# Optimization experiments

Measured on AMD Instinct MI355X. Metric: run time of the kernel, lower is better.

Reference implementation:

```python
import jax, jax.numpy as jnp
import numpy as np

N = 50000      # nodes
E = 400000     # edges (before self-loops)
DIN = 128
HID = 128
HEADS = 4
DOUT = 64
NEG_SLOPE = 0.2  # PyG GATConv default


def setup_inputs() -> dict:
    key = jax.random.key(0)
    ks = jax.random.split(key, 14)

    def w(k, shape, fan_in):
        return jax.random.normal(k, shape, dtype=jnp.float32) * (1.0 / np.sqrt(fan_in))

    x = jax.random.normal(ks[0], (N, DIN), dtype=jnp.float32)
    edge_index = jax.random.randint(ks[1], (2, E), 0, N, dtype=jnp.int32)

    # layer 1: DIN -> HEADS*HID (concat)
    W1 = w(ks[2], (DIN, HEADS * HID), DIN)
    a_src1 = w(ks[3], (HEADS, HID), HID)
    a_dst1 = w(ks[4], (HEADS, HID), HID)
    b1 = jnp.zeros((HEADS * HID,), jnp.float32)
    # layer 2: HEADS*HID -> HEADS*HID (concat)
    W2 = w(ks[5], (HEADS * HID, HEADS * HID), HEADS * HID)
    a_src2 = w(ks[6], (HEADS, HID), HID)
    a_dst2 = w(ks[7], (HEADS, HID), HID)
    b2 = jnp.zeros((HEADS * HID,), jnp.float32)
    # layer 3: HEADS*HID -> DOUT, heads=1, concat=False (mean)
    W3 = w(ks[8], (HEADS * HID, DOUT), HEADS * HID)
    a_src3 = w(ks[9], (1, DOUT), DOUT)
    a_dst3 = w(ks[10], (1, DOUT), DOUT)
    b3 = jnp.zeros((DOUT,), jnp.float32)

    return dict(x=x, edge_index=edge_index,
                W1=W1, a_src1=a_src1, a_dst1=a_dst1, b1=b1,
                W2=W2, a_src2=a_src2, a_dst2=a_dst2, b2=b2,
                W3=W3, a_src3=a_src3, a_dst3=a_dst3, b3=b3)


def _gat_layer(x, src, dst, W, a_src, a_dst, n):
    """One GATConv (eval mode, self-loops already in src/dst). Returns [n, H, C]."""
    H, C = a_src.shape
    h = (x @ W).reshape(n, H, C)                        # projected features
    alpha_s = jnp.einsum('nhc,hc->nh', h, a_src)        # per-node src logits
    alpha_d = jnp.einsum('nhc,hc->nh', h, a_dst)
    e = jax.nn.leaky_relu(alpha_s[src] + alpha_d[dst], NEG_SLOPE)  # [E', H]
    # segment softmax over incoming edges of each dst node
    m = jax.ops.segment_max(e, dst, num_segments=n)
    e = jnp.exp(e - m[dst])
    s = jax.ops.segment_sum(e, dst, num_segments=n)
    alpha = e / (s[dst] + 1e-16)                        # [E', H]
    msg = h[src] * alpha[:, :, None]                    # [E', H, C]
    return jax.ops.segment_sum(msg, dst, num_segments=n)


def reference(x, edge_index, W1, a_src1, a_dst1, b1,
              W2, a_src2, a_dst2, b2, W3, a_src3, a_dst3, b3):
    n = x.shape[0]
    loops = jnp.arange(n, dtype=edge_index.dtype)       # PyG add_self_loops=True
    src = jnp.concatenate([edge_index[0], loops])
    dst = jnp.concatenate([edge_index[1], loops])

    h = _gat_layer(x, src, dst, W1, a_src1, a_dst1, n).reshape(n, -1) + b1
    h = jax.nn.elu(h)   # dropout is identity in eval mode
    h = _gat_layer(h, src, dst, W2, a_src2, a_dst2, n).reshape(n, -1) + b2
    h = jax.nn.elu(h)
    out = _gat_layer(h, src, dst, W3, a_src3, a_dst3, n)[:, 0, :] + b3  # heads=1, concat=False
    return out
```

## Files before the change

kernel.cpp:

```cpp
#include <hip/hip_runtime.h>
#include <hip/hip_bf16.h>


typedef __attribute__((ext_vector_type(8))) short bf16x8;
typedef __attribute__((ext_vector_type(4))) float f32x4;

__device__ __forceinline__ float bflo(unsigned w) { return __uint_as_float(w << 16); }
__device__ __forceinline__ float bfhi(unsigned w) { return __uint_as_float(w & 0xffff0000u); }
__device__ __forceinline__ float leaky(float x) { return x > 0.f ? x : 0.2f * x; }
__device__ __forceinline__ unsigned pack2(float a, float b) {
    unsigned ua = __bfloat16_as_ushort(__float2bfloat16(a));
    unsigned ub = __bfloat16_as_ushort(__float2bfloat16(b));
    return ua | (ub << 16);
}


__global__ void k_count(const int* __restrict__ ei, int E, int N, int* __restrict__ cnt) {
    int e = blockIdx.x * blockDim.x + threadIdx.x;
    int tot = E + N;
    if (e >= tot) return;
    int d = (e < E) ? ei[E + e] : (e - E);
    atomicAdd(&cnt[d], 1);
}

__global__ void k_scan1(const int* __restrict__ cnt, int N, int* __restrict__ rp,
                        int* __restrict__ blksum) {
    __shared__ int sdata[256];
    int t = threadIdx.x;
    int base = blockIdx.x * 1024;
    int v[4];
    int loc = 0;
#pragma unroll
    for (int i = 0; i < 4; i++) {
        int idx = base + t * 4 + i;
        v[i] = (idx < N) ? ((cnt[idx] + 3) & ~3) : 0;
        loc += v[i];
    }
    int x = loc;
    sdata[t] = x;
    __syncthreads();
    for (int off = 1; off < 256; off <<= 1) {
        int y = (t >= off) ? sdata[t - off] : 0;
        __syncthreads();
        x += y;
        sdata[t] = x;
        __syncthreads();
    }
    int run = x - loc;
#pragma unroll
    for (int i = 0; i < 4; i++) {
        int idx = base + t * 4 + i;
        if (idx < N) rp[idx] = run;
        run += v[i];
    }
    if (t == 255) blksum[blockIdx.x] = x;
}

__global__ void k_scan2(const int* __restrict__ blksum, int nblk, int* __restrict__ blkoff) {
    int l = threadIdx.x;
    int v = (l < nblk) ? blksum[l] : 0;
    int x = v;
#pragma unroll
    for (int off = 1; off < 64; off <<= 1) {
        int y = __shfl_up(x, off);
        if (l >= off) x += y;
    }
    if (l < nblk) blkoff[l] = x - v;
}

__global__ void k_scan3(int* __restrict__ rp, const int* __restrict__ blkoff,
                        const int* __restrict__ blksum, const int* __restrict__ cnt,
                        int N, int nblk, int* __restrict__ cur,
                        int* __restrict__ col, int* __restrict__ dste) {
    int i = blockIdx.x * blockDim.x + threadIdx.x;
    if (i < N) {
        int v = rp[i] + blkoff[i >> 10];
        rp[i] = v;
        cur[i] = v;
        int c = cnt[i];
        int pad = ((c + 3) & ~3) - c;
        for (int p = 0; p < pad; p++) {
            col[v + c + p] = 0;
            dste[v + c + p] = -1;
        }
    }
    if (i == 0) rp[N] = blkoff[nblk - 1] + blksum[nblk - 1];
}

__global__ void k_fill(const int* __restrict__ ei, int E, int N, int* __restrict__ cur,
                       int* __restrict__ col, int* __restrict__ dste) {
    int e = blockIdx.x * blockDim.x + threadIdx.x;
    int tot = E + N;
    if (e >= tot) return;
    int s, d;
    if (e < E) { s = ei[e]; d = ei[E + e]; }
    else       { s = e - E; d = e - E; }
    int p = atomicAdd(&cur[d], 1);
    col[p] = s;
    dste[p] = d;
}


__global__ void k_cast_pad(const float* __restrict__ X, __hip_bfloat16* __restrict__ Xb,
                           int n_elems, int total) {
    int i = (blockIdx.x * blockDim.x + threadIdx.x) * 4;
    if (i >= total) return;
    float4 v = make_float4(0.f, 0.f, 0.f, 0.f);
    if (i < n_elems) v = *(const float4*)&X[i];
    __hip_bfloat16 tmp[4] = {__float2bfloat16(v.x), __float2bfloat16(v.y),
                             __float2bfloat16(v.z), __float2bfloat16(v.w)};
    *(ushort4*)&Xb[i] = *(const ushort4*)tmp;
}

__global__ void k_castT(const float* __restrict__ W, __hip_bfloat16* __restrict__ Wt,
                        int K, int Nw) {
    __shared__ float t[32][33];
    int k0 = blockIdx.x * 32, n0 = blockIdx.y * 32;
    int tx = threadIdx.x & 31, ty = threadIdx.x >> 5;
    for (int i = ty; i < 32; i += 8) t[i][tx] = W[(size_t)(k0 + i) * Nw + n0 + tx];
    __syncthreads();
    for (int i = ty; i < 32; i += 8)
        Wt[(size_t)(n0 + i) * K + k0 + tx] = __float2bfloat16(t[tx][i]);
}

__global__ void k_va1(const float* __restrict__ W1, const float* __restrict__ asrc,
                      const float* __restrict__ adst, float* __restrict__ va8) {
    int t = threadIdx.x;
    int c = t >> 2, h = t & 3;
    const float* wrow = W1 + (size_t)c * 512 + h * 128;
    const float* av = asrc + h * 128;
    const float* dv = adst + h * 128;
    float vs = 0.f, vd = 0.f;
    for (int k = 0; k < 128; k++) {
        float wv = wrow[k];
        vs += wv * av[k];
        vd += wv * dv[k];
    }
    va8[c * 8 + h] = vs;
    va8[c * 8 + 4 + h] = vd;
}

__global__ void k_alpha_x(const __hip_bfloat16* __restrict__ xb,
                          const float* __restrict__ va8, float* __restrict__ as_out,
                          float* __restrict__ ad_out, int N) {
    int w = (blockIdx.x * blockDim.x + threadIdx.x) >> 6;
    int lane = threadIdx.x & 63;
    if (w >= N) return;
    unsigned wrd = ((const unsigned*)xb)[(size_t)w * 64 + lane];
    float f0 = bflo(wrd), f1 = bfhi(wrd);
    int c0 = lane * 2;
    float4 vs0 = *(const float4*)&va8[c0 * 8];
    float4 vd0 = *(const float4*)&va8[c0 * 8 + 4];
    float4 vs1 = *(const float4*)&va8[(c0 + 1) * 8];
    float4 vd1 = *(const float4*)&va8[(c0 + 1) * 8 + 4];
    float s[8];
    s[0] = f0 * vs0.x + f1 * vs1.x;
    s[1] = f0 * vs0.y + f1 * vs1.y;
    s[2] = f0 * vs0.z + f1 * vs1.z;
    s[3] = f0 * vs0.w + f1 * vs1.w;
    s[4] = f0 * vd0.x + f1 * vd1.x;
    s[5] = f0 * vd0.y + f1 * vd1.y;
    s[6] = f0 * vd0.z + f1 * vd1.z;
    s[7] = f0 * vd0.w + f1 * vd1.w;
#pragma unroll
    for (int off = 32; off >= 1; off >>= 1)
#pragma unroll
        for (int j = 0; j < 8; j++) s[j] += __shfl_xor(s[j], off);
    if (lane == 0) {
        *(float4*)&as_out[w * 4] = make_float4(s[0], s[1], s[2], s[3]);
        *(float4*)&ad_out[w * 4] = make_float4(s[4], s[5], s[6], s[7]);
    }
}


template <int BM, int BN, bool FUSE>
__global__ void __launch_bounds__(256) k_gemm_mfma(const __hip_bfloat16* __restrict__ A,
                                                   const __hip_bfloat16* __restrict__ Bt,
                                                   __hip_bfloat16* __restrict__ C,
                                                   int lda, int ldc, int K,
                                                   int hsA, int hsB, int hsC,
                                                   const float* __restrict__ bias) {
    constexpr int BK = 64;
    constexpr int WM = BM / 2;
    constexpr int WN = BN / 2;
    constexpr int MREP = WM / 16;
    constexpr int NREP = WN / 16;

    __shared__ __hip_bfloat16 lds[(BM + BN) * BK];
    __hip_bfloat16* As = lds;
    __hip_bfloat16* Bs = lds + BM * BK;

    const int z = blockIdx.z;
    A += (size_t)z * hsA;
    Bt += (size_t)z * hsB;
    const int cbase = z * hsC;

    const int tid = threadIdx.x;
    const int wave = tid >> 6;
    const int lane = tid & 63;
    const int wm0 = (wave >> 1) * WM;
    const int wn0 = (wave & 1) * WN;
    const int m0 = blockIdx.y * BM;
    const int n0 = blockIdx.x * BN;
    const int fr = lane & 15;
    const int fq = lane >> 4;

    f32x4 acc[MREP][NREP] = {};

    for (int kt = 0; kt < K; kt += BK) {
        const __hip_bfloat16* srcA = A + (size_t)m0 * lda + kt;
#pragma unroll
        for (int it = 0; it < BM * 8 / 256; ++it) {
            int gb = it * 256 + wave * 64;
            int g = gb + lane;
            int row = g >> 3;
            int kg = (g & 7) ^ (row & 7);
            const __hip_bfloat16* gsrc = srcA + (size_t)row * lda + kg * 8;
            __builtin_amdgcn_global_load_lds(
                (const __attribute__((address_space(1))) void*)gsrc,
                (__attribute__((address_space(3))) void*)(As + gb * 8), 16, 0, 0);
        }
        const __hip_bfloat16* srcB = Bt + (size_t)n0 * K + kt;
#pragma unroll
        for (int it = 0; it < BN * 8 / 256; ++it) {
            int gb = it * 256 + wave * 64;
            int g = gb + lane;
            int row = g >> 3;
            int kg = (g & 7) ^ (row & 7);
            const __hip_bfloat16* gsrc = srcB + (size_t)row * K + kg * 8;
            __builtin_amdgcn_global_load_lds(
                (const __attribute__((address_space(1))) void*)gsrc,
                (__attribute__((address_space(3))) void*)(Bs + gb * 8), 16, 0, 0);
        }
        __syncthreads();

#pragma unroll
        for (int sl = 0; sl < 2; ++sl) {
            int ke = sl * 32 + fq * 8;
            bf16x8 af[MREP], bfr[NREP];
#pragma unroll
            for (int i = 0; i < MREP; ++i) {
                int row = wm0 + i * 16 + fr;
                int e = (row * BK + ke) ^ ((row & 7) << 3);
                af[i] = *(const bf16x8*)(As + e);
            }
#pragma unroll
            for (int j = 0; j < NREP; ++j) {
                int row = wn0 + j * 16 + fr;
                int e = (row * BK + ke) ^ ((row & 7) << 3);
                bfr[j] = *(const bf16x8*)(Bs + e);
            }
#pragma unroll
            for (int i = 0; i < MREP; ++i)
#pragma unroll
                for (int j = 0; j < NREP; ++j)
                    acc[i][j] = __builtin_amdgcn_mfma_f32_16x16x32_bf16(
                        af[i], bfr[j], acc[i][j], 0, 0, 0);
        }
        __syncthreads();
    }

#pragma unroll
    for (int i = 0; i < MREP; ++i) {
#pragma unroll
        for (int j = 0; j < NREP; ++j) {
            int colg = cbase + n0 + wn0 + j * 16 + fr;
#pragma unroll
            for (int r = 0; r < 4; ++r) {
                int rowg = m0 + wm0 + i * 16 + fq * 4 + r;
                float v = acc[i][j][r];
                if (FUSE) {
                    v += bias[colg];
                    v = v > 0.f ? v : expm1f(v);
                }
                C[(size_t)rowg * ldc + colg] = __float2bfloat16(v);
            }
        }
    }
}


template <int C, int H>
__global__ void k_alpha(const __hip_bfloat16* __restrict__ h, const float* __restrict__ a_src,
                        const float* __restrict__ a_dst, float* __restrict__ as_out,
                        float* __restrict__ ad_out, int N) {
    int w = (blockIdx.x * blockDim.x + threadIdx.x) >> 6;
    int lane = threadIdx.x & 63;
    int n = w / H, hd = w % H;
    if (n >= N) return;
    const __hip_bfloat16* hp = h + (size_t)n * (C * H) + hd * C;
    const float* asp = a_src + hd * C;
    const float* adp = a_dst + hd * C;
    float s1 = 0.f, s2 = 0.f;
    if constexpr (C == 128) {
        unsigned wrd = *(const unsigned*)(hp + 2 * lane);
        float f0 = bflo(wrd), f1 = bfhi(wrd);
        float2 a2 = *(const float2*)(asp + 2 * lane);
        float2 d2 = *(const float2*)(adp + 2 * lane);
        s1 = f0 * a2.x + f1 * a2.y;
        s2 = f0 * d2.x + f1 * d2.y;
    } else {
        float v = __bfloat162float(hp[lane & 63]);
        s1 = v * asp[lane];
        s2 = v * adp[lane];
    }
#pragma unroll
    for (int off = 32; off >= 1; off >>= 1) {
        s1 += __shfl_xor(s1, off);
        s2 += __shfl_xor(s2, off);
    }
    if (lane == 0) {
        as_out[n * H + hd] = s1;
        ad_out[n * H + hd] = s2;
    }
}


__global__ void k_edgewA(const int* __restrict__ col, const int* __restrict__ dste,
                         const float* __restrict__ as, const float* __restrict__ ad,
                         float* __restrict__ wA, const int* __restrict__ rp, int N) {
    int e = blockIdx.x * blockDim.x + threadIdx.x;
    if (e >= rp[N]) return;
    int d = dste[e];
    if (d < 0) {
        *(float4*)&wA[e * 4] = make_float4(0.f, 0.f, 0.f, 0.f);
        return;
    }
    int s = col[e];
    float4 a = *(const float4*)&as[s * 4];
    float4 b = *(const float4*)&ad[d * 4];
    float4 w;
    w.x = __expf(leaky(a.x + b.x));
    w.y = __expf(leaky(a.y + b.y));
    w.z = __expf(leaky(a.z + b.z));
    w.w = __expf(leaky(a.w + b.w));
    *(float4*)&wA[e * 4] = w;
}


__global__ void k_gatherX(const __hip_bfloat16* __restrict__ xb,
                          const float* __restrict__ wA, const int* __restrict__ rp,
                          const int* __restrict__ col, unsigned* __restrict__ out32, int N) {
    int w = (blockIdx.x * blockDim.x + threadIdx.x) >> 6;
    int lane = threadIdx.x & 63;
    if (w >= N) return;
    int d = w;
    int r0 = rp[d], r1 = rp[d + 1];
    const unsigned* xp = (const unsigned*)xb;

    float acc[8] = {};
    float ws0 = 0.f, ws1 = 0.f, ws2 = 0.f, ws3 = 0.f;
    for (int e = r0; e < r1; e += 4) {
        int4 c4 = *(const int4*)&col[e];
        float4 w0 = *(const float4*)&wA[e * 4];
        float4 w1 = *(const float4*)&wA[e * 4 + 4];
        float4 w2 = *(const float4*)&wA[e * 4 + 8];
        float4 w3 = *(const float4*)&wA[e * 4 + 12];
        unsigned v0 = xp[(size_t)c4.x * 64 + lane];
        unsigned v1 = xp[(size_t)c4.y * 64 + lane];
        unsigned v2 = xp[(size_t)c4.z * 64 + lane];
        unsigned v3 = xp[(size_t)c4.w * 64 + lane];
        ws0 += w0.x + w1.x + w2.x + w3.x;
        ws1 += w0.y + w1.y + w2.y + w3.y;
        ws2 += w0.z + w1.z + w2.z + w3.z;
        ws3 += w0.w + w1.w + w2.w + w3.w;
        float f0, f1;
        f0 = bflo(v0); f1 = bfhi(v0);
        acc[0] += w0.x * f0; acc[1] += w0.x * f1;
        acc[2] += w0.y * f0; acc[3] += w0.y * f1;
        acc[4] += w0.z * f0; acc[5] += w0.z * f1;
        acc[6] += w0.w * f0; acc[7] += w0.w * f1;
        f0 = bflo(v1); f1 = bfhi(v1);
        acc[0] += w1.x * f0; acc[1] += w1.x * f1;
        acc[2] += w1.y * f0; acc[3] += w1.y * f1;
        acc[4] += w1.z * f0; acc[5] += w1.z * f1;
        acc[6] += w1.w * f0; acc[7] += w1.w * f1;
        f0 = bflo(v2); f1 = bfhi(v2);
        acc[0] += w2.x * f0; acc[1] += w2.x * f1;
        acc[2] += w2.y * f0; acc[3] += w2.y * f1;
        acc[4] += w2.z * f0; acc[5] += w2.z * f1;
        acc[6] += w2.w * f0; acc[7] += w2.w * f1;
        f0 = bflo(v3); f1 = bfhi(v3);
        acc[0] += w3.x * f0; acc[1] += w3.x * f1;
        acc[2] += w3.y * f0; acc[3] += w3.y * f1;
        acc[4] += w3.z * f0; acc[5] += w3.z * f1;
        acc[6] += w3.w * f0; acc[7] += w3.w * f1;
    }
    float i0 = 1.f / (ws0 + 1e-16f), i1 = 1.f / (ws1 + 1e-16f);
    float i2 = 1.f / (ws2 + 1e-16f), i3 = 1.f / (ws3 + 1e-16f);
    size_t ob = (size_t)d * 256 + lane;
    out32[ob]       = pack2(acc[0] * i0, acc[1] * i0);
    out32[ob + 64]  = pack2(acc[2] * i1, acc[3] * i1);
    out32[ob + 128] = pack2(acc[4] * i2, acc[5] * i2);
    out32[ob + 192] = pack2(acc[6] * i3, acc[7] * i3);
}


template <bool DO_ELU>
__global__ void k_gather512(const __hip_bfloat16* __restrict__ hfeat,
                            const float* __restrict__ as4, const float* __restrict__ ad4,
                            const int* __restrict__ cnt, const int* __restrict__ rp,
                            const int* __restrict__ col, const float* __restrict__ bias,
                            __hip_bfloat16* __restrict__ out, int N) {
    int w = (blockIdx.x * blockDim.x + threadIdx.x) >> 6;
    int lane = threadIdx.x & 63;
    if (w >= N) return;
    int d = w;
    int r0 = rp[d], r1 = rp[d + 1];
    int r1r = r0 + cnt[d];
    int hd = lane >> 4;
    float adv = ad4[d * 4 + hd];
    const uint4* hp = (const uint4*)hfeat;

    float acc[8] = {};
    float wsum = 0.f;
    for (int e = r0; e < r1; e += 4) {
        int4 c4 = *(const int4*)&col[e];
        float l0 = as4[c4.x * 4 + hd] + adv;
        float l1 = as4[c4.y * 4 + hd] + adv;
        float l2 = as4[c4.z * 4 + hd] + adv;
        float l3 = as4[c4.w * 4 + hd] + adv;
        uint4 v0 = hp[(size_t)c4.x * 64 + lane];
        uint4 v1 = hp[(size_t)c4.y * 64 + lane];
        uint4 v2 = hp[(size_t)c4.z * 64 + lane];
        uint4 v3 = hp[(size_t)c4.w * 64 + lane];
        float w0 = (e + 0 < r1r) ? __expf(leaky(l0)) : 0.f;
        float w1 = (e + 1 < r1r) ? __expf(leaky(l1)) : 0.f;
        float w2 = (e + 2 < r1r) ? __expf(leaky(l2)) : 0.f;
        float w3 = (e + 3 < r1r) ? __expf(leaky(l3)) : 0.f;
        wsum += (w0 + w1) + (w2 + w3);
        acc[0] += w0 * bflo(v0.x); acc[1] += w0 * bfhi(v0.x);
        acc[2] += w0 * bflo(v0.y); acc[3] += w0 * bfhi(v0.y);
        acc[4] += w0 * bflo(v0.z); acc[5] += w0 * bfhi(v0.z);
        acc[6] += w0 * bflo(v0.w); acc[7] += w0 * bfhi(v0.w);
        acc[0] += w1 * bflo(v1.x); acc[1] += w1 * bfhi(v1.x);
        acc[2] += w1 * bflo(v1.y); acc[3] += w1 * bfhi(v1.y);
        acc[4] += w1 * bflo(v1.z); acc[5] += w1 * bfhi(v1.z);
        acc[6] += w1 * bflo(v1.w); acc[7] += w1 * bfhi(v1.w);
        acc[0] += w2 * bflo(v2.x); acc[1] += w2 * bfhi(v2.x);
        acc[2] += w2 * bflo(v2.y); acc[3] += w2 * bfhi(v2.y);
        acc[4] += w2 * bflo(v2.z); acc[5] += w2 * bfhi(v2.z);
        acc[6] += w2 * bflo(v2.w); acc[7] += w2 * bfhi(v2.w);
        acc[0] += w3 * bflo(v3.x); acc[1] += w3 * bfhi(v3.x);
        acc[2] += w3 * bflo(v3.y); acc[3] += w3 * bfhi(v3.y);
        acc[4] += w3 * bflo(v3.z); acc[5] += w3 * bfhi(v3.z);
        acc[6] += w3 * bflo(v3.w); acc[7] += w3 * bfhi(v3.w);
    }

    float inv = 1.0f / (wsum + 1e-16f);
    __hip_bfloat16 tmp[8];
#pragma unroll
    for (int j = 0; j < 8; j++) {
        float v = acc[j] * inv + bias[lane * 8 + j];
        if (DO_ELU) v = v > 0.f ? v : expm1f(v);
        tmp[j] = __float2bfloat16(v);
    }
    *(float4*)(out + (size_t)d * 512 + lane * 8) = *(const float4*)tmp;
}


__global__ void k_gather64(const __hip_bfloat16* __restrict__ hfeat,
                           const float* __restrict__ as1, const float* __restrict__ ad1,
                           const int* __restrict__ cnt, const int* __restrict__ rp,
                           const int* __restrict__ col, const float* __restrict__ bias,
                           float* __restrict__ out, int N) {
    int w = (blockIdx.x * blockDim.x + threadIdx.x) >> 6;
    int lane = threadIdx.x & 63;
    if (w >= N) return;
    int d = w;
    int r0 = rp[d], r1 = rp[d + 1];
    int r1r = r0 + cnt[d];
    float adv = ad1[d];
    int g = lane >> 4, cl = lane & 15;

    float a0 = 0.f, a1 = 0.f, a2 = 0.f, a3 = 0.f, wsum = 0.f;
    for (int e0 = r0; e0 < r1; e0 += 4) {
        int e = e0 + g;
        int s = col[e];
        float l = as1[s] + adv;
        uint2 q = *(const uint2*)(hfeat + (size_t)s * 64 + cl * 4);
        float wf = (e < r1r) ? __expf(leaky(l)) : 0.f;
        wsum += wf;
        a0 += wf * bflo(q.x);
        a1 += wf * bfhi(q.x);
        a2 += wf * bflo(q.y);
        a3 += wf * bfhi(q.y);
    }
#pragma unroll
    for (int off = 16; off <= 32; off <<= 1) {
        a0 += __shfl_xor(a0, off);
        a1 += __shfl_xor(a1, off);
        a2 += __shfl_xor(a2, off);
        a3 += __shfl_xor(a3, off);
        wsum += __shfl_xor(wsum, off);
    }
    if (g == 0) {
        float inv = 1.0f / (wsum + 1e-16f);
        float4 b4 = *(const float4*)&bias[cl * 4];
        float4 o = make_float4(a0 * inv + b4.x, a1 * inv + b4.y,
                               a2 * inv + b4.z, a3 * inv + b4.w);
        *(float4*)(out + (size_t)d * 64 + cl * 4) = o;
    }
}


extern "C" void kernel_launch(void* const* d_in, const int* in_sizes, int n_in,
                              void* d_out, int out_size, void* d_ws, size_t ws_size,
                              hipStream_t stream) {
    const float* x   = (const float*)d_in[0];
    const int*   ei  = (const int*)d_in[1];
    const float* W1  = (const float*)d_in[2];
    const float* as1 = (const float*)d_in[3];
    const float* ad1 = (const float*)d_in[4];
    const float* b1  = (const float*)d_in[5];
    const float* W2  = (const float*)d_in[6];
    const float* as2 = (const float*)d_in[7];
    const float* ad2 = (const float*)d_in[8];
    const float* b2  = (const float*)d_in[9];
    const float* W3  = (const float*)d_in[10];
    const float* as3 = (const float*)d_in[11];
    const float* ad3 = (const float*)d_in[12];
    const float* b3  = (const float*)d_in[13];

    const int N = in_sizes[0] / 128;
    const int E = in_sizes[1] / 2;
    const int Etot = E + N;
    const int EP = (Etot + 3 * N + 255) & ~255;
    const int Mp = (N + 127) & ~127;

    char* ws = (char*)d_ws;
    size_t off = 0;
    auto alloc = [&](size_t bytes) -> void* {
        void* p = ws + off;
        off = (off + bytes + 255) & ~(size_t)255;
        return p;
    };
    __hip_bfloat16* hbuf = (__hip_bfloat16*)alloc((size_t)Mp * 512 * 2);
    __hip_bfloat16* fbuf = (__hip_bfloat16*)alloc((size_t)Mp * 512 * 2);
    __hip_bfloat16* xagg = (__hip_bfloat16*)alloc((size_t)Mp * 512 * 2);
    __hip_bfloat16* xb   = (__hip_bfloat16*)alloc((size_t)Mp * 128 * 2);
    __hip_bfloat16* Wt1  = (__hip_bfloat16*)alloc((size_t)512 * 128 * 2);
    __hip_bfloat16* Wt2  = (__hip_bfloat16*)alloc((size_t)512 * 512 * 2);
    __hip_bfloat16* Wt3  = (__hip_bfloat16*)alloc((size_t)64 * 512 * 2);
    float* aS   = (float*)alloc((size_t)N * 4 * 4);
    float* aD   = (float*)alloc((size_t)N * 4 * 4);
    float* wbuf = (float*)alloc((size_t)EP * 4 * 4);
    float* va8  = (float*)alloc(128 * 8 * 4);
    int* cnt  = (int*)alloc((size_t)N * 4);
    int* rp   = (int*)alloc((size_t)(N + 1) * 4);
    int* cur  = (int*)alloc((size_t)N * 4);
    int* col  = (int*)alloc((size_t)EP * 4);
    int* dste = (int*)alloc((size_t)EP * 4);
    int* blks = (int*)alloc(64 * 4);
    int* blko = (int*)alloc(64 * 4);

    hipMemsetAsync(cnt, 0, (size_t)N * 4, stream);
    int thr = 256;
    k_count<<<(Etot + thr - 1) / thr, thr, 0, stream>>>(ei, E, N, cnt);
    int nblk = (N + 1023) / 1024;
    k_scan1<<<nblk, 256, 0, stream>>>(cnt, N, rp, blks);
    k_scan2<<<1, 64, 0, stream>>>(blks, nblk, blko);
    k_scan3<<<(N + 255) / 256, 256, 0, stream>>>(rp, blko, blks, cnt, N, nblk, cur, col, dste);
    k_fill<<<(Etot + thr - 1) / thr, thr, 0, stream>>>(ei, E, N, cur, col, dste);

    {
        int total = Mp * 128;
        k_cast_pad<<<(total / 4 + 255) / 256, 256, 0, stream>>>(x, xb, N * 128, total);
        dim3 g1(128 / 32, 512 / 32);
        k_castT<<<g1, 256, 0, stream>>>(W1, Wt1, 128, 512);
        dim3 g2(512 / 32, 512 / 32);
        k_castT<<<g2, 256, 0, stream>>>(W2, Wt2, 512, 512);
        dim3 g3(512 / 32, 64 / 32);
        k_castT<<<g3, 256, 0, stream>>>(W3, Wt3, 512, 64);
        k_va1<<<1, 512, 0, stream>>>(W1, as1, ad1, va8);
    }

    int alphaBlocks4 = (int)(((size_t)N * 4 * 64 + 255) / 256);
    int alphaBlocks1 = (int)(((size_t)N * 64 + 255) / 256);
    int edgeBlocks = (EP + 255) / 256;
    int gatBlocks = (N + 3) / 4;

    k_alpha_x<<<gatBlocks, 256, 0, stream>>>(xb, va8, aS, aD, N);
    k_edgewA<<<edgeBlocks, 256, 0, stream>>>(col, dste, aS, aD, wbuf, rp, N);
    k_gatherX<<<gatBlocks, 256, 0, stream>>>(xb, wbuf, rp, col, (unsigned*)xagg, N);
    {
        dim3 g(1, Mp / 128, 4);
        k_gemm_mfma<128, 128, true><<<g, 256, 0, stream>>>(xagg, Wt1, fbuf,
                                                           512, 512, 128,
                                                           128, 128 * 128, 128, b1);
    }

    {
        dim3 g(4, Mp / 128, 1);
        k_gemm_mfma<128, 128, false><<<g, 256, 0, stream>>>(fbuf, Wt2, hbuf,
                                                            512, 512, 512, 0, 0, 0, nullptr);
    }
    k_alpha<128, 4><<<alphaBlocks4, 256, 0, stream>>>(hbuf, as2, ad2, aS, aD, N);
    k_gather512<true><<<gatBlocks, 256, 0, stream>>>(hbuf, aS, aD, cnt, rp, col, b2, fbuf, N);

    {
        dim3 g(1, Mp / 64, 1);
        k_gemm_mfma<64, 64, false><<<g, 256, 0, stream>>>(fbuf, Wt3, hbuf,
                                                          512, 64, 512, 0, 0, 0, nullptr);
    }
    k_alpha<64, 1><<<alphaBlocks1, 256, 0, stream>>>(hbuf, as3, ad3, aS, aD, N);
    k_gather64<<<gatBlocks, 256, 0, stream>>>(hbuf, aS, aD, cnt, rp, col, b3,
                                              (float*)d_out, N);
}
```

Baseline: 408.2 us.

## Fuse attention-logit computation into GEMM epilogue and layer-2 gather

Removes the two standalone k_alpha passes. Layer-2 src/dst logits are now reduced from the MFMA accumulators in the GEMM epilogue, with a cross-wave combine through LDS. Layer-3 logits come from the layer-2 gather output dotted with precomputed W3·a vectors (k_va3). This avoids re-reading the projected features from memory, at the cost of extra epilogue work and shuffles. The layer-3 logits are now taken from pre-quantization fp32 values rather than from the bf16 GEMM output.

```diff
diff --git a/kernel.cpp b/kernel.cpp
--- a/kernel.cpp
+++ b/kernel.cpp
@@ -138,6 +138,21 @@
     }
     va8[c * 8 + h] = vs;
     va8[c * 8 + 4 + h] = vd;
+}
+
+__global__ void k_va3(const float* __restrict__ W3, const float* __restrict__ asrc,
+                      const float* __restrict__ adst, float* __restrict__ va3s,
+                      float* __restrict__ va3d) {
+    int c = threadIdx.x;
+    const float* wrow = W3 + (size_t)c * 64;
+    float vs = 0.f, vd = 0.f;
+    for (int k = 0; k < 64; k++) {
+        float wv = wrow[k];
+        vs += wv * asrc[k];
+        vd += wv * adst[k];
+    }
+    va3s[c] = vs;
+    va3d[c] = vd;
 }
 
 __global__ void k_alpha_x(const __hip_bfloat16* __restrict__ xb,
@@ -173,13 +188,17 @@
 }
 
 
-template <int BM, int BN, bool FUSE>
+template <int BM, int BN, bool FUSE, bool ALPHA>
 __global__ void __launch_bounds__(256) k_gemm_mfma(const __hip_bfloat16* __restrict__ A,
                                                    const __hip_bfloat16* __restrict__ Bt,
                                                    __hip_bfloat16* __restrict__ C,
                                                    int lda, int ldc, int K,
                                                    int hsA, int hsB, int hsC,
-                                                   const float* __restrict__ bias) {
+                                                   const float* __restrict__ bias,
+                                                   const float* __restrict__ aSrcTab,
+                                                   const float* __restrict__ aDstTab,
+                                                   float* __restrict__ asOut,
+                                                   float* __restrict__ adOut) {
     constexpr int BK = 64;
     constexpr int WM = BM / 2;
     constexpr int WN = BN / 2;
@@ -277,41 +296,60 @@
             }
         }
     }
-}
-
-
-template <int C, int H>
-__global__ void k_alpha(const __hip_bfloat16* __restrict__ h, const float* __restrict__ a_src,
-                        const float* __restrict__ a_dst, float* __restrict__ as_out,
-                        float* __restrict__ ad_out, int N) {
-    int w = (blockIdx.x * blockDim.x + threadIdx.x) >> 6;
-    int lane = threadIdx.x & 63;
-    int n = w / H, hd = w % H;
-    if (n >= N) return;
-    const __hip_bfloat16* hp = h + (size_t)n * (C * H) + hd * C;
-    const float* asp = a_src + hd * C;
-    const float* adp = a_dst + hd * C;
-    float s1 = 0.f, s2 = 0.f;
-    if constexpr (C == 128) {
-        unsigned wrd = *(const unsigned*)(hp + 2 * lane);
-        float f0 = bflo(wrd), f1 = bfhi(wrd);
-        float2 a2 = *(const float2*)(asp + 2 * lane);
-        float2 d2 = *(const float2*)(adp + 2 * lane);
-        s1 = f0 * a2.x + f1 * a2.y;
-        s2 = f0 * d2.x + f1 * d2.y;
-    } else {
-        float v = __bfloat162float(hp[lane & 63]);
-        s1 = v * asp[lane];
-        s2 = v * adp[lane];
-    }
-#pragma unroll
-    for (int off = 32; off >= 1; off >>= 1) {
-        s1 += __shfl_xor(s1, off);
-        s2 += __shfl_xor(s2, off);
-    }
-    if (lane == 0) {
-        as_out[n * H + hd] = s1;
-        ad_out[n * H + hd] = s2;
+
+    if constexpr (ALPHA) {
+        const int head = blockIdx.x;
+        float avs[NREP], avd[NREP];
+#pragma unroll
+        for (int j = 0; j < NREP; ++j) {
+            int cl = wn0 + j * 16 + fr;
+            avs[j] = aSrcTab[head * 128 + cl];
+            avd[j] = aDstTab[head * 128 + cl];
+        }
+        float pa[MREP][4] = {};
+        float pd_[MREP][4] = {};
+#pragma unroll
+        for (int i = 0; i < MREP; ++i)
+#pragma unroll
+            for (int j = 0; j < NREP; ++j)
+#pragma unroll
+                for (int r = 0; r < 4; ++r) {
+                    pa[i][r] += acc[i][j][r] * avs[j];
+                    pd_[i][r] += acc[i][j][r] * avd[j];
+                }
+#pragma unroll
+        for (int off = 1; off <= 8; off <<= 1)
+#pragma unroll
+            for (int i = 0; i < MREP; ++i)
+#pragma unroll
+                for (int r = 0; r < 4; ++r) {
+                    pa[i][r] += __shfl_xor(pa[i][r], off);
+                    pd_[i][r] += __shfl_xor(pd_[i][r], off);
+                }
+        float* lds_a = (float*)lds;
+        float* lds_d = lds_a + BM;
+        if ((wave & 1) == 0 && fr == 0) {
+#pragma unroll
+            for (int i = 0; i < MREP; ++i)
+#pragma unroll
+                for (int r = 0; r < 4; ++r) {
+                    int rl = wm0 + i * 16 + fq * 4 + r;
+                    lds_a[rl] = pa[i][r];
+                    lds_d[rl] = pd_[i][r];
+                }
+        }
+        __syncthreads();
+        if ((wave & 1) == 1 && fr == 0) {
+#pragma unroll
+            for (int i = 0; i < MREP; ++i)
+#pragma unroll
+                for (int r = 0; r < 4; ++r) {
+                    int rl = wm0 + i * 16 + fq * 4 + r;
+                    int rowg = m0 + rl;
+                    asOut[rowg * 4 + head] = lds_a[rl] + pa[i][r];
+                    adOut[rowg * 4 + head] = lds_d[rl] + pd_[i][r];
+                }
+        }
     }
 }
 
@@ -401,7 +439,9 @@
                             const float* __restrict__ as4, const float* __restrict__ ad4,
                             const int* __restrict__ cnt, const int* __restrict__ rp,
                             const int* __restrict__ col, const float* __restrict__ bias,
-                            __hip_bfloat16* __restrict__ out, int N) {
+                            __hip_bfloat16* __restrict__ out,
+                            const float* __restrict__ va3s, const float* __restrict__ va3d,
+                            float* __restrict__ as3, float* __restrict__ ad3, int N) {
     int w = (blockIdx.x * blockDim.x + threadIdx.x) >> 6;
     int lane = threadIdx.x & 63;
     if (w >= N) return;
@@ -448,14 +488,32 @@
     }
 
     float inv = 1.0f / (wsum + 1e-16f);
+    float vals[8];
     __hip_bfloat16 tmp[8];
 #pragma unroll
     for (int j = 0; j < 8; j++) {
         float v = acc[j] * inv + bias[lane * 8 + j];
         if (DO_ELU) v = v > 0.f ? v : expm1f(v);
+        vals[j] = v;
         tmp[j] = __float2bfloat16(v);
     }
     *(float4*)(out + (size_t)d * 512 + lane * 8) = *(const float4*)tmp;
+
+    float s3 = 0.f, d3 = 0.f;
+#pragma unroll
+    for (int j = 0; j < 8; j++) {
+        s3 += vals[j] * va3s[lane * 8 + j];
+        d3 += vals[j] * va3d[lane * 8 + j];
+    }
+#pragma unroll
+    for (int off = 32; off >= 1; off >>= 1) {
+        s3 += __shfl_xor(s3, off);
+        d3 += __shfl_xor(d3, off);
+    }
+    if (lane == 0) {
+        as3[d] = s3;
+        ad3[d] = d3;
+    }
 }
 
 
@@ -542,10 +600,14 @@
     __hip_bfloat16* Wt1  = (__hip_bfloat16*)alloc((size_t)512 * 128 * 2);
     __hip_bfloat16* Wt2  = (__hip_bfloat16*)alloc((size_t)512 * 512 * 2);
     __hip_bfloat16* Wt3  = (__hip_bfloat16*)alloc((size_t)64 * 512 * 2);
-    float* aS   = (float*)alloc((size_t)N * 4 * 4);
-    float* aD   = (float*)alloc((size_t)N * 4 * 4);
+    float* aS   = (float*)alloc((size_t)Mp * 4 * 4);
+    float* aD   = (float*)alloc((size_t)Mp * 4 * 4);
+    float* aS3  = (float*)alloc((size_t)Mp * 4);
+    float* aD3  = (float*)alloc((size_t)Mp * 4);
     float* wbuf = (float*)alloc((size_t)EP * 4 * 4);
     float* va8  = (float*)alloc(128 * 8 * 4);
+    float* va3s = (float*)alloc(512 * 4);
+    float* va3d = (float*)alloc(512 * 4);
     int* cnt  = (int*)alloc((size_t)N * 4);
     int* rp   = (int*)alloc((size_t)(N + 1) * 4);
     int* cur  = (int*)alloc((size_t)N * 4);
@@ -573,10 +635,9 @@
         dim3 g3(512 / 32, 64 / 32);
         k_castT<<<g3, 256, 0, stream>>>(W3, Wt3, 512, 64);
         k_va1<<<1, 512, 0, stream>>>(W1, as1, ad1, va8);
-    }
-
-    int alphaBlocks4 = (int)(((size_t)N * 4 * 64 + 255) / 256);
-    int alphaBlocks1 = (int)(((size_t)N * 64 + 255) / 256);
+        k_va3<<<1, 512, 0, stream>>>(W3, as3, ad3, va3s, va3d);
+    }
+
     int edgeBlocks = (EP + 255) / 256;
     int gatBlocks = (N + 3) / 4;
 
@@ -585,25 +646,26 @@
     k_gatherX<<<gatBlocks, 256, 0, stream>>>(xb, wbuf, rp, col, (unsigned*)xagg, N);
     {
         dim3 g(1, Mp / 128, 4);
-        k_gemm_mfma<128, 128, true><<<g, 256, 0, stream>>>(xagg, Wt1, fbuf,
-                                                           512, 512, 128,
-                                                           128, 128 * 128, 128, b1);
+        k_gemm_mfma<128, 128, true, false><<<g, 256, 0, stream>>>(
+            xagg, Wt1, fbuf, 512, 512, 128, 128, 128 * 128, 128, b1,
+            nullptr, nullptr, nullptr, nullptr);
     }
 
     {
         dim3 g(4, Mp / 128, 1);
-        k_gemm_mfma<128, 128, false><<<g, 256, 0, stream>>>(fbuf, Wt2, hbuf,
-                                                            512, 512, 512, 0, 0, 0, nullptr);
-    }
-    k_alpha<128, 4><<<alphaBlocks4, 256, 0, stream>>>(hbuf, as2, ad2, aS, aD, N);
-    k_gather512<true><<<gatBlocks, 256, 0, stream>>>(hbuf, aS, aD, cnt, rp, col, b2, fbuf, N);
+        k_gemm_mfma<128, 128, false, true><<<g, 256, 0, stream>>>(
+            fbuf, Wt2, hbuf, 512, 512, 512, 0, 0, 0, nullptr,
+            as2, ad2, aS, aD);
+    }
+    k_gather512<true><<<gatBlocks, 256, 0, stream>>>(hbuf, aS, aD, cnt, rp, col, b2,
+                                                     fbuf, va3s, va3d, aS3, aD3, N);
 
     {
         dim3 g(1, Mp / 64, 1);
-        k_gemm_mfma<64, 64, false><<<g, 256, 0, stream>>>(fbuf, Wt3, hbuf,
-                                                          512, 64, 512, 0, 0, 0, nullptr);
-    }
-    k_alpha<64, 1><<<alphaBlocks1, 256, 0, stream>>>(hbuf, as3, ad3, aS, aD, N);
-    k_gather64<<<gatBlocks, 256, 0, stream>>>(hbuf, aS, aD, cnt, rp, col, b3,
+        k_gemm_mfma<64, 64, false, false><<<g, 256, 0, stream>>>(
+            fbuf, Wt3, hbuf, 512, 64, 512, 0, 0, 0, nullptr,
+            nullptr, nullptr, nullptr, nullptr);
+    }
+    k_gather64<<<gatBlocks, 256, 0, stream>>>(hbuf, aS3, aD3, cnt, rp, col, b3,
                                               (float*)d_out, N);
 }
```

Result: no change. 400.3 us (-1.9%).
